# Performance work log

Hardware: AMD Instinct MI355X
Metric: run time of the kernel (lower is better)

## Reference

```python
import jax, jax.numpy as jnp
import numpy as np

B, S, DM = 4, 2048, 512
H, D = 8, 64          # att_head, head_dim = att_dim // att_head
LEFT, RIGHT = 128, 128  # band_part(left_mask, right_mask)
LARGE = 1e30          # masked_softmax large number for fp32


def setup_inputs() -> dict:
    key = jax.random.key(0)
    ks = jax.random.split(key, 11)
    scale = 1.0 / np.sqrt(DM)
    x = jax.random.normal(ks[0], (B, S, DM), jnp.float32)
    Wq = jax.random.normal(ks[1], (DM, DM), jnp.float32) * scale
    bq = jnp.zeros((DM,), jnp.float32)
    Wk = jax.random.normal(ks[2], (DM, DM), jnp.float32) * scale
    bk = jnp.zeros((DM,), jnp.float32)
    Wv = jax.random.normal(ks[3], (DM, DM), jnp.float32) * scale
    bv = jnp.zeros((DM,), jnp.float32)
    Wo = jax.random.normal(ks[4], (DM, DM), jnp.float32) * scale
    bo = jnp.zeros((DM,), jnp.float32)
    x_len = jax.random.randint(ks[5], (B,), 0, 2048)
    return {"x": x, "Wq": Wq, "bq": bq, "Wk": Wk, "bk": bk,
            "Wv": Wv, "bv": bv, "Wo": Wo, "bo": bo, "x_len": x_len}


def reference(x, Wq, bq, Wk, bk, Wv, bv, Wo, bo, x_len):
    b, s, _ = x.shape
    # QKV projections, split into heads: [B,S,H,D]
    q = (x @ Wq + bq).reshape(b, s, H, D)
    k = (x @ Wk + bk).reshape(b, s, H, D)
    v = (x @ Wv + bv).reshape(b, s, H, D)
    # content energy: [B,H,Q,K], scaled by sqrt(head_dim)
    energy = jnp.einsum('bind,bjnd->bnij', q, k) / jnp.sqrt(jnp.float32(D))
    # banded mask (tf.linalg.band_part semantics): keep -LEFT <= j-i <= RIGHT
    i = jnp.arange(s)[:, None]
    j = jnp.arange(s)[None, :]
    band = ((j - i) <= RIGHT) & ((i - j) <= LEFT)            # [S,S]
    # key-length mask (tf.sequence_mask, expanded to [B,1,1,S])
    seq = jnp.arange(s)[None, :] < x_len[:, None]            # [B,S]
    mask = (band[None, None, :, :] & seq[:, None, None, :]).astype(energy.dtype)
    # masked softmax: energy - (1 - mask) * LARGE, softmax over keys
    att = jax.nn.softmax(energy - (1.0 - mask) * LARGE, axis=-1)
    # context: [B,Q,H,D] -> [B,S,H*D]
    ctx = jnp.einsum('bnij,bjnd->bind', att, v).reshape(b, s, H * D)
    # output projection (use_proj=True)
    return ctx @ Wo + bo
```

## Files before the change

kernel.cpp:

```cpp
#include <hip/hip_runtime.h>

#define S_LEN 2048
#define BATCH 4
#define DMODEL 512
#define NHEAD 8
#define HDIM 64
#define ROWS (BATCH * S_LEN)

using short8 = __attribute__((ext_vector_type(8))) short;
using f32x4  = __attribute__((ext_vector_type(4))) float;

__device__ __forceinline__ unsigned short f2bf(float f) {
  unsigned int u = __builtin_bit_cast(unsigned int, f);
  u += 0x7fffu + ((u >> 16) & 1u);
  return (unsigned short)(u >> 16);
}
__device__ __forceinline__ float bf2f(unsigned short h) {
  unsigned int u = ((unsigned int)h) << 16;
  return __builtin_bit_cast(float, u);
}
__device__ __forceinline__ void glds16(const void* g, void* l) {
  __builtin_amdgcn_global_load_lds((const __attribute__((address_space(1))) unsigned*)g,
                                   (__attribute__((address_space(3))) unsigned*)l, 16, 0, 0);
}

__global__ __launch_bounds__(256) void prep_kernel(const float* __restrict__ x,
                                                   const float* __restrict__ Wq,
                                                   const float* __restrict__ Wk,
                                                   const float* __restrict__ Wv,
                                                   const float* __restrict__ Wo,
                                                   unsigned short* __restrict__ xb,
                                                   unsigned short* __restrict__ WqkT,
                                                   unsigned short* __restrict__ WvT,
                                                   unsigned short* __restrict__ WoT,
                                                   float* __restrict__ xpart) {
  __shared__ float t[32][33];
  const int blk = blockIdx.x, tid = threadIdx.x;
  if (blk < 2048) {
    const int base = (blk * 256 + tid) * 8;
    float4 f0 = *(const float4*)(x + base);
    float4 f1 = *(const float4*)(x + base + 4);
    uint4 o;
    o.x = (unsigned)f2bf(f0.x) | ((unsigned)f2bf(f0.y) << 16);
    o.y = (unsigned)f2bf(f0.z) | ((unsigned)f2bf(f0.w) << 16);
    o.z = (unsigned)f2bf(f1.x) | ((unsigned)f2bf(f1.y) << 16);
    o.w = (unsigned)f2bf(f1.z) | ((unsigned)f2bf(f1.w) << 16);
    *(uint4*)(xb + base) = o;
    return;
  }
  if (blk < 3072) {
    const int tb = blk - 2048;
    const int which = tb >> 8, tile = tb & 255;
    const float* W = which == 0 ? Wq : which == 1 ? Wk : which == 2 ? Wv : Wo;
    unsigned short* WT = which == 0 ? WqkT : which == 1 ? (WqkT + 512 * 512)
                        : which == 2 ? WvT : WoT;
    const int tx = tid & 31, ty = tid >> 5;
    const int x0 = (tile & 15) * 32, y0 = (tile >> 4) * 32;
#pragma unroll
    for (int r = 0; r < 4; r++)
      t[ty + 8 * r][tx] = W[(size_t)(y0 + ty + 8 * r) * DMODEL + x0 + tx];
    __syncthreads();
#pragma unroll
    for (int r = 0; r < 4; r++)
      WT[(size_t)(x0 + ty + 8 * r) * DMODEL + y0 + tx] = f2bf(t[tx][ty + 8 * r]);
    return;
  }
  const int u = blk - 3072;
  const int b = u >> 4, cg = (u >> 3) & 1, rc = u & 7;
  const float* base = x + (size_t)(b * S_LEN + rc * 256) * DMODEL + cg * 256 + tid;
  float s = 0.f;
  for (int j = 0; j < 256; j++) s += base[(size_t)j * DMODEL];
  xpart[u * 256 + tid] = s;
}

__global__ __launch_bounds__(256, 2) void qkv_kernel(const unsigned short* __restrict__ xb,
                                                     const unsigned short* __restrict__ WqkT,
                                                     const unsigned short* __restrict__ WvT,
                                                     const float* __restrict__ bq,
                                                     const float* __restrict__ bk,
                                                     const float* __restrict__ bv,
                                                     const int* __restrict__ x_len,
                                                     const float* __restrict__ xpart,
                                                     unsigned short* __restrict__ Qb,
                                                     unsigned short* __restrict__ Kb,
                                                     unsigned short* __restrict__ Vt,
                                                     float* __restrict__ vsum) {
  __shared__ __align__(16) char smem[32768];
  const int bid = blockIdx.x;
  const int tid = threadIdx.x;
  const int wave = tid >> 6, lane = tid & 63;
  if (bid >= 768) {
    const int u = bid - 768;
    const int b = u >> 5;
    const int cg = lane >> 5, ko = (lane & 31) * 8;
    float xs[8] = {};
#pragma unroll
    for (int rc = 0; rc < 8; rc++) {
      const float* p = xpart + ((b * 16 + cg * 8 + rc) << 8) + ko;
      float4 a0 = *(const float4*)p;
      float4 a1 = *(const float4*)(p + 4);
      xs[0] += a0.x; xs[1] += a0.y; xs[2] += a0.z; xs[3] += a0.w;
      xs[4] += a1.x; xs[5] += a1.y; xs[6] += a1.z; xs[7] += a1.w;
    }
#pragma unroll
    for (int ci = 0; ci < 4; ci++) {
      const int f = (u & 31) * 16 + wave * 4 + ci;
      const uint4 wv = *(const uint4*)(WvT + (size_t)f * DMODEL + lane * 8);
      const unsigned int w[4] = {wv.x, wv.y, wv.z, wv.w};
      float acc = 0.f;
#pragma unroll
      for (int e = 0; e < 4; e++) {
        acc += xs[2 * e] * bf2f((unsigned short)(w[e] & 0xffffu));
        acc += xs[2 * e + 1] * bf2f((unsigned short)(w[e] >> 16));
      }
#pragma unroll
      for (int off = 1; off < 64; off <<= 1) acc += __shfl_xor(acc, off, 64);
      if (lane == 0) vsum[b * DMODEL + f] = acc + 2048.f * bv[f];
    }
    return;
  }
  const bool vmode = bid < 256;
  const unsigned short *A, *Bt;
  int m0, n0;
  if (vmode) {
    m0 = (bid & 3) * 128;
    n0 = (bid >> 2) * 128;
    A = WvT; Bt = xb;
    if ((n0 & 2047) >= x_len[n0 >> 11]) return;
  } else {
    const int q = bid - 256;
    m0 = (q >> 3) * 128;
    n0 = (q & 7) * 128;
    A = xb; Bt = WqkT;
    const int xl = x_len[m0 >> 11];
    const int s0 = m0 & 2047;
    if (n0 >= DMODEL) { if (s0 >= xl) return; }
    else if (s0 >= xl + 128) return;
  }
  char* As = smem;
  char* Bs = smem + 16384;
  const int wr = wave >> 1, wc = wave & 1;
  const int lm = lane & 15, lq = lane >> 4;
  const int srow = lane >> 3;
  const int slc = (lane & 7) ^ (srow & 7);
  const unsigned short* gA[4];
  const unsigned short* gB[4];
  char *lA[4], *lB[4];
#pragma unroll
  for (int i = 0; i < 4; i++) {
    const int g = wave * 4 + i;
    gA[i] = A + (size_t)(m0 + g * 8 + srow) * DMODEL + slc * 8;
    gB[i] = Bt + (size_t)(n0 + g * 8 + srow) * DMODEL + slc * 8;
    lA[i] = As + g * 1024 + lane * 16;
    lB[i] = Bs + g * 1024 + lane * 16;
  }
  int aoff[4][2], boff[4][2];
#pragma unroll
  for (int mi = 0; mi < 4; mi++)
#pragma unroll
    for (int h = 0; h < 2; h++) {
      aoff[mi][h] = (wr * 64 + mi * 16 + lm) * 128 + ((((h << 2) | lq)) ^ (lm & 7)) * 16;
      boff[mi][h] = (wc * 64 + mi * 16 + lm) * 128 + ((((h << 2) | lq)) ^ (lm & 7)) * 16;
    }
  f32x4 acc[4][4] = {};
  for (int k0 = 0; k0 < DMODEL; k0 += 64) {
    __syncthreads();
#pragma unroll
    for (int i = 0; i < 4; i++) {
      glds16(gA[i] + k0, lA[i]);
      glds16(gB[i] + k0, lB[i]);
    }
    __syncthreads();
#pragma unroll
    for (int h = 0; h < 2; h++) {
      short8 af[4], bfr[4];
#pragma unroll
      for (int mi = 0; mi < 4; mi++) af[mi] = *(const short8*)(As + aoff[mi][h]);
#pragma unroll
      for (int ni = 0; ni < 4; ni++) bfr[ni] = *(const short8*)(Bs + boff[ni][h]);
#pragma unroll
      for (int mi = 0; mi < 4; mi++)
#pragma unroll
        for (int ni = 0; ni < 4; ni++)
          acc[mi][ni] = __builtin_amdgcn_mfma_f32_16x16x32_bf16(af[mi], bfr[ni], acc[mi][ni], 0, 0, 0);
    }
  }
#pragma unroll
  for (int mi = 0; mi < 4; mi++) {
    const int row0 = m0 + wr * 64 + mi * 16 + lq * 4;
#pragma unroll
    for (int ni = 0; ni < 4; ni++) {
      const int col = n0 + wc * 64 + ni * 16 + lm;
#pragma unroll
      for (int r = 0; r < 4; r++) {
        const int row = row0 + r;
        const float v = acc[mi][ni][r];
        if (vmode) {
          Vt[(size_t)row * ROWS + col] = f2bf(v + bv[row]);
        } else if (col < DMODEL) {
          Qb[(size_t)row * DMODEL + col] = f2bf(v + bq[col]);
        } else {
          Kb[(size_t)row * DMODEL + (col - DMODEL)] = f2bf(v + bk[col - DMODEL]);
        }
      }
    }
  }
}

__global__ __launch_bounds__(256) void attn_kernel(const unsigned short* __restrict__ Q,
                                                   const unsigned short* __restrict__ K,
                                                   const unsigned short* __restrict__ Vt,
                                                   const int* __restrict__ x_len,
                                                   const float* __restrict__ vsum,
                                                   const unsigned short* __restrict__ WoT,
                                                   const float* __restrict__ bo,
                                                   float* __restrict__ trow,
                                                   unsigned short* __restrict__ ctx) {
  __shared__ unsigned short Ks[64][72];
  __shared__ unsigned short Vs[64][72];
  __shared__ unsigned short Ps[4][16][72];
  const int tid = threadIdx.x;
  const int unit = blockIdx.x;
  const int wave = tid >> 6, lane = tid & 63;
  if (unit >= 1024) {
    const int u = unit - 1024;
    const int b = u >> 4;
    const float* vs = vsum + b * DMODEL + lane * 8;
    float vreg[8];
    *(float4*)vreg = *(const float4*)vs;
    *(float4*)(vreg + 4) = *(const float4*)(vs + 4);
#pragma unroll
    for (int ci = 0; ci < 8; ci++) {
      const int c = (u & 15) * 32 + wave * 8 + ci;
      const uint4 wv = *(const uint4*)(WoT + (size_t)c * DMODEL + lane * 8);
      const unsigned int w[4] = {wv.x, wv.y, wv.z, wv.w};
      float acc = 0.f;
#pragma unroll
      for (int e = 0; e < 4; e++) {
        acc += vreg[2 * e] * bf2f((unsigned short)(w[e] & 0xffffu));
        acc += vreg[2 * e + 1] * bf2f((unsigned short)(w[e] >> 16));
      }
#pragma unroll
      for (int off = 1; off < 64; off <<= 1) acc += __shfl_xor(acc, off, 64);
      if (lane == 0) trow[b * DMODEL + c] = bo[c] + acc * (1.f / 2048.f);
    }
    return;
  }
  const int b = unit >> 8, h = (unit >> 5) & 7;
  const int i0 = (unit & 31) * 64;
  const int xlen = x_len[b];
  const int t0 = min(S_LEN, xlen + 128);
  if ((i0 & ~127) >= t0) return;
  const int lm = lane & 15, lq = lane >> 4;
  const int q0 = i0 + wave * 16;
  const size_t qoff = (size_t)(b * S_LEN + q0 + lm) * DMODEL + h * HDIM + lq * 8;
  const short8 aq0 = *(const short8*)(Q + qoff);
  const short8 aq1 = *(const short8*)(Q + qoff + 32);
  const int sr = tid >> 3, sc = (tid & 7) * 8;
  f32x4 oacc[4] = {};
  float lrow[4] = {0.f, 0.f, 0.f, 0.f};
  for (int kt = 0; kt < 5; kt++) {
    const int jt0 = i0 - 128 + kt * 64;
    if (jt0 + 63 < 0 || jt0 >= xlen) continue;
    __syncthreads();
    {
      const int jr0 = min(max(jt0 + sr, 0), S_LEN - 1);
      const int jr1 = min(max(jt0 + sr + 32, 0), S_LEN - 1);
      *(uint4*)&Ks[sr][sc] =
          *(const uint4*)(K + (size_t)(b * S_LEN + jr0) * DMODEL + h * HDIM + sc);
      *(uint4*)&Ks[sr + 32][sc] =
          *(const uint4*)(K + (size_t)(b * S_LEN + jr1) * DMODEL + h * HDIM + sc);
      const int jvc = min(max(jt0 + sc, 0), S_LEN - 8);
      *(uint4*)&Vs[sr][sc] =
          *(const uint4*)(Vt + (size_t)(h * HDIM + sr) * ROWS + b * S_LEN + jvc);
      *(uint4*)&Vs[sr + 32][sc] =
          *(const uint4*)(Vt + (size_t)(h * HDIM + sr + 32) * ROWS + b * S_LEN + jvc);
    }
    __syncthreads();
    if (jt0 + 63 < q0 - 128 || jt0 > q0 + 143) continue;

    f32x4 sv[4];
#pragma unroll
    for (int sub = 0; sub < 4; sub++) {
      const short8 bk0 = *(const short8*)&Ks[sub * 16 + lm][lq * 8];
      const short8 bk1 = *(const short8*)&Ks[sub * 16 + lm][32 + lq * 8];
      f32x4 s = {};
      s = __builtin_amdgcn_mfma_f32_16x16x32_bf16(aq0, bk0, s, 0, 0, 0);
      s = __builtin_amdgcn_mfma_f32_16x16x32_bf16(aq1, bk1, s, 0, 0, 0);
      sv[sub] = s;
    }
    float p[4][4];
#pragma unroll
    for (int sub = 0; sub < 4; sub++) {
      const int j = jt0 + sub * 16 + lm;
      const bool jv = (j >= 0) && (j < xlen);
#pragma unroll
      for (int r = 0; r < 4; r++) {
        const int i = q0 + lq * 4 + r;
        const bool ok = jv && (j - i <= 128) && (i - j <= 128);
        const float pv = ok ? __expf(sv[sub][r] * 0.125f) : 0.f;
        p[sub][r] = pv;
        lrow[r] += pv;
      }
    }
#pragma unroll
    for (int sub = 0; sub < 4; sub++)
#pragma unroll
      for (int r = 0; r < 4; r++)
        Ps[wave][lq * 4 + r][sub * 16 + lm] = f2bf(p[sub][r]);
    const short8 pf0 = *(const short8*)&Ps[wave][lm][lq * 8];
    const short8 pf1 = *(const short8*)&Ps[wave][lm][32 + lq * 8];
#pragma unroll
    for (int dt = 0; dt < 4; dt++) {
      const short8 bv0 = *(const short8*)&Vs[dt * 16 + lm][lq * 8];
      const short8 bv1 = *(const short8*)&Vs[dt * 16 + lm][32 + lq * 8];
      oacc[dt] = __builtin_amdgcn_mfma_f32_16x16x32_bf16(pf0, bv0, oacc[dt], 0, 0, 0);
      oacc[dt] = __builtin_amdgcn_mfma_f32_16x16x32_bf16(pf1, bv1, oacc[dt], 0, 0, 0);
    }
  }
#pragma unroll
  for (int r = 0; r < 4; r++)
#pragma unroll
    for (int off = 1; off < 16; off <<= 1) lrow[r] += __shfl_xor(lrow[r], off, 64);
#pragma unroll
  for (int r = 0; r < 4; r++) {
    const int i = q0 + lq * 4 + r;
    const size_t obase = (size_t)(b * S_LEN + i) * DMODEL + h * HDIM;
    if (lrow[r] > 0.f) {
      const float inv = 1.f / lrow[r];
#pragma unroll
      for (int dt = 0; dt < 4; dt++)
        ctx[obase + dt * 16 + lm] = f2bf(oacc[dt][r] * inv);
    } else {
#pragma unroll
      for (int dt = 0; dt < 4; dt++)
        ctx[obase + dt * 16 + lm] =
            f2bf(vsum[(size_t)b * DMODEL + h * HDIM + dt * 16 + lm] * (1.f / 2048.f));
    }
  }
}

__global__ __launch_bounds__(256, 2) void out_kernel(const unsigned short* __restrict__ A,
                                                     const unsigned short* __restrict__ Bt,
                                                     const float* __restrict__ bias,
                                                     const int* __restrict__ x_len,
                                                     const float* __restrict__ trow,
                                                     float* __restrict__ out) {
  __shared__ __align__(16) char smem[32768];
  const int tid = threadIdx.x;
  const int m0 = (blockIdx.x >> 2) * 128, n0 = (blockIdx.x & 3) * 128;
  const int xl = x_len[m0 >> 11];
  if ((m0 & 2047) >= min(S_LEN, xl + 128)) {
    const float4 val = *(const float4*)(trow + (m0 >> 11) * DMODEL + n0 + (tid & 31) * 4);
    float* obase = out + (size_t)m0 * DMODEL + n0 + (tid & 31) * 4;
#pragma unroll
    for (int r = tid >> 5; r < 128; r += 8)
      *(float4*)(obase + (size_t)r * DMODEL) = val;
    return;
  }
  char* As = smem;
  char* Bs = smem + 16384;
  const int wave = tid >> 6, lane = tid & 63;
  const int wr = wave >> 1, wc = wave & 1;
  const int lm = lane & 15, lq = lane >> 4;
  const int srow = lane >> 3;
  const int slc = (lane & 7) ^ (srow & 7);
  const unsigned short* gA[4];
  const unsigned short* gB[4];
  char *lA[4], *lB[4];
#pragma unroll
  for (int i = 0; i < 4; i++) {
    const int g = wave * 4 + i;
    gA[i] = A + (size_t)(m0 + g * 8 + srow) * DMODEL + slc * 8;
    gB[i] = Bt + (size_t)(n0 + g * 8 + srow) * DMODEL + slc * 8;
    lA[i] = As + g * 1024 + lane * 16;
    lB[i] = Bs + g * 1024 + lane * 16;
  }
  int aoff[4][2], boff[4][2];
#pragma unroll
  for (int mi = 0; mi < 4; mi++)
#pragma unroll
    for (int h = 0; h < 2; h++) {
      aoff[mi][h] = (wr * 64 + mi * 16 + lm) * 128 + ((((h << 2) | lq)) ^ (lm & 7)) * 16;
      boff[mi][h] = (wc * 64 + mi * 16 + lm) * 128 + ((((h << 2) | lq)) ^ (lm & 7)) * 16;
    }
  f32x4 acc[4][4] = {};
  for (int k0 = 0; k0 < DMODEL; k0 += 64) {
    __syncthreads();
#pragma unroll
    for (int i = 0; i < 4; i++) {
      glds16(gA[i] + k0, lA[i]);
      glds16(gB[i] + k0, lB[i]);
    }
    __syncthreads();
#pragma unroll
    for (int h = 0; h < 2; h++) {
      short8 af[4], bfr[4];
#pragma unroll
      for (int mi = 0; mi < 4; mi++) af[mi] = *(const short8*)(As + aoff[mi][h]);
#pragma unroll
      for (int ni = 0; ni < 4; ni++) bfr[ni] = *(const short8*)(Bs + boff[ni][h]);
#pragma unroll
      for (int mi = 0; mi < 4; mi++)
#pragma unroll
        for (int ni = 0; ni < 4; ni++)
          acc[mi][ni] = __builtin_amdgcn_mfma_f32_16x16x32_bf16(af[mi], bfr[ni], acc[mi][ni], 0, 0, 0);
    }
  }
#pragma unroll
  for (int mi = 0; mi < 4; mi++) {
    const int row0 = m0 + wr * 64 + mi * 16 + lq * 4;
#pragma unroll
    for (int ni = 0; ni < 4; ni++) {
      const int col = n0 + wc * 64 + ni * 16 + lm;
#pragma unroll
      for (int r = 0; r < 4; r++)
        out[(size_t)(row0 + r) * DMODEL + col] = acc[mi][ni][r] + bias[col];
    }
  }
}

extern "C" void kernel_launch(void* const* d_in, const int* in_sizes, int n_in,
                              void* d_out, int out_size, void* d_ws, size_t ws_size,
                              hipStream_t stream) {
  (void)in_sizes; (void)n_in; (void)out_size; (void)ws_size;
  const float* x  = (const float*)d_in[0];
  const float* Wq = (const float*)d_in[1];
  const float* bq = (const float*)d_in[2];
  const float* Wk = (const float*)d_in[3];
  const float* bk = (const float*)d_in[4];
  const float* Wv = (const float*)d_in[5];
  const float* bv = (const float*)d_in[6];
  const float* Wo = (const float*)d_in[7];
  const float* bo = (const float*)d_in[8];
  const int* x_len = (const int*)d_in[9];

  char* ws = (char*)d_ws;
  const size_t MB = 1024 * 1024;
  unsigned short* xb   = (unsigned short*)(ws + 0 * MB);
  unsigned short* Qb   = (unsigned short*)(ws + 8 * MB);
  unsigned short* Kb   = (unsigned short*)(ws + 16 * MB);
  unsigned short* Vt   = (unsigned short*)(ws + 24 * MB);
  unsigned short* Cx   = (unsigned short*)(ws + 32 * MB);
  unsigned short* WqkT = (unsigned short*)(ws + 40 * MB);
  unsigned short* WvT  = (unsigned short*)(ws + 41 * MB);
  unsigned short* WoT  = (unsigned short*)(ws + 41 * MB + 512 * 1024);
  float* vsum          = (float*)(ws + 42 * MB);
  float* trow          = (float*)(ws + 42 * MB + 8192);
  float* xpart         = (float*)(ws + 43 * MB);

  prep_kernel<<<3136, 256, 0, stream>>>(x, Wq, Wk, Wv, Wo, xb, WqkT, WvT, WoT, xpart);
  qkv_kernel<<<896, 256, 0, stream>>>(xb, WqkT, WvT, bq, bk, bv, x_len, xpart,
                                      Qb, Kb, Vt, vsum);
  attn_kernel<<<1088, 256, 0, stream>>>(Qb, Kb, Vt, x_len, vsum, WoT, bo, trow, Cx);
  out_kernel<<<256, 256, 0, stream>>>(Cx, WoT, bo, x_len, trow, (float*)d_out);
}
```

Measured before the change: 146.8 us.

## Double-buffer GEMM and attention K/V tiles to overlap loads with MFMA

The QKV and output GEMMs now use a K-step of 32 with two shared-memory buffers, so the next tile's global-to-LDS loads are issued before the MFMAs on the current tile, and there is one barrier per step instead of two. The attention kernel double-buffers K and V tiles, prefetching the next tile into registers while computing on the current one, and computes the valid key-tile range up front instead of skipping tiles inside the loop. qkv launch bounds are raised to 3 blocks per CU. The change hides memory latency at the cost of more LDS and register use and a new swizzle that must stay correct.

```diff
diff --git a/kernel.cpp b/kernel.cpp
--- a/kernel.cpp
+++ b/kernel.cpp
@@ -73,7 +73,7 @@
   xpart[u * 256 + tid] = s;
 }
 
-__global__ __launch_bounds__(256, 2) void qkv_kernel(const unsigned short* __restrict__ xb,
+__global__ __launch_bounds__(256, 3) void qkv_kernel(const unsigned short* __restrict__ xb,
                                                      const unsigned short* __restrict__ WqkT,
                                                      const unsigned short* __restrict__ WvT,
                                                      const float* __restrict__ bq,
@@ -137,53 +137,50 @@
     if (n0 >= DMODEL) { if (s0 >= xl) return; }
     else if (s0 >= xl + 128) return;
   }
-  char* As = smem;
-  char* Bs = smem + 16384;
   const int wr = wave >> 1, wc = wave & 1;
   const int lm = lane & 15, lq = lane >> 4;
-  const int srow = lane >> 3;
-  const int slc = (lane & 7) ^ (srow & 7);
-  const unsigned short* gA[4];
-  const unsigned short* gB[4];
-  char *lA[4], *lB[4];
-#pragma unroll
-  for (int i = 0; i < 4; i++) {
-    const int g = wave * 4 + i;
-    gA[i] = A + (size_t)(m0 + g * 8 + srow) * DMODEL + slc * 8;
-    gB[i] = Bt + (size_t)(n0 + g * 8 + srow) * DMODEL + slc * 8;
-    lA[i] = As + g * 1024 + lane * 16;
-    lB[i] = Bs + g * 1024 + lane * 16;
-  }
-  int aoff[4][2], boff[4][2];
-#pragma unroll
-  for (int mi = 0; mi < 4; mi++)
-#pragma unroll
-    for (int h = 0; h < 2; h++) {
-      aoff[mi][h] = (wr * 64 + mi * 16 + lm) * 128 + ((((h << 2) | lq)) ^ (lm & 7)) * 16;
-      boff[mi][h] = (wc * 64 + mi * 16 + lm) * 128 + ((((h << 2) | lq)) ^ (lm & 7)) * 16;
-    }
+  const int r4 = tid >> 2;
+  const int cl = (tid & 3) ^ ((tid >> 3) & 3);
+  const unsigned short* ga0 = A + (size_t)(m0 + r4) * DMODEL + cl * 8;
+  const unsigned short* ga1 = ga0 + (size_t)64 * DMODEL;
+  const unsigned short* gb0 = Bt + (size_t)(n0 + r4) * DMODEL + cl * 8;
+  const unsigned short* gb1 = gb0 + (size_t)64 * DMODEL;
+  char* la0 = smem + tid * 16;
+  char* lb0 = smem + 16384 + tid * 16;
+  const int phys = (lq ^ ((lm >> 1) & 3)) * 16;
+  int aoff[4], boff[4];
+#pragma unroll
+  for (int mi = 0; mi < 4; mi++) {
+    aoff[mi] = (wr * 64 + mi * 16 + lm) * 64 + phys;
+    boff[mi] = (wc * 64 + mi * 16 + lm) * 64 + phys;
+  }
   f32x4 acc[4][4] = {};
-  for (int k0 = 0; k0 < DMODEL; k0 += 64) {
-    __syncthreads();
-#pragma unroll
-    for (int i = 0; i < 4; i++) {
-      glds16(gA[i] + k0, lA[i]);
-      glds16(gB[i] + k0, lB[i]);
-    }
-    __syncthreads();
-#pragma unroll
-    for (int h = 0; h < 2; h++) {
-      short8 af[4], bfr[4];
-#pragma unroll
-      for (int mi = 0; mi < 4; mi++) af[mi] = *(const short8*)(As + aoff[mi][h]);
-#pragma unroll
-      for (int ni = 0; ni < 4; ni++) bfr[ni] = *(const short8*)(Bs + boff[ni][h]);
-#pragma unroll
-      for (int mi = 0; mi < 4; mi++)
-#pragma unroll
-        for (int ni = 0; ni < 4; ni++)
-          acc[mi][ni] = __builtin_amdgcn_mfma_f32_16x16x32_bf16(af[mi], bfr[ni], acc[mi][ni], 0, 0, 0);
-    }
+  glds16(ga0, la0);
+  glds16(ga1, la0 + 4096);
+  glds16(gb0, lb0);
+  glds16(gb1, lb0 + 4096);
+  __syncthreads();
+#pragma unroll
+  for (int it = 0; it < 16; ++it) {
+    if (it < 15) {
+      const int nb = ((it + 1) & 1) << 13;
+      glds16(ga0 + (it + 1) * 32, la0 + nb);
+      glds16(ga1 + (it + 1) * 32, la0 + nb + 4096);
+      glds16(gb0 + (it + 1) * 32, lb0 + nb);
+      glds16(gb1 + (it + 1) * 32, lb0 + nb + 4096);
+    }
+    const int ab = (it & 1) << 13;
+    short8 af[4], bfr[4];
+#pragma unroll
+    for (int mi = 0; mi < 4; mi++) af[mi] = *(const short8*)(smem + ab + aoff[mi]);
+#pragma unroll
+    for (int ni = 0; ni < 4; ni++) bfr[ni] = *(const short8*)(smem + 16384 + ab + boff[ni]);
+#pragma unroll
+    for (int mi = 0; mi < 4; mi++)
+#pragma unroll
+      for (int ni = 0; ni < 4; ni++)
+        acc[mi][ni] = __builtin_amdgcn_mfma_f32_16x16x32_bf16(af[mi], bfr[ni], acc[mi][ni], 0, 0, 0);
+    if (it < 15) __syncthreads();
   }
 #pragma unroll
   for (int mi = 0; mi < 4; mi++) {
@@ -216,8 +213,8 @@
                                                    const float* __restrict__ bo,
                                                    float* __restrict__ trow,
                                                    unsigned short* __restrict__ ctx) {
-  __shared__ unsigned short Ks[64][72];
-  __shared__ unsigned short Vs[64][72];
+  __shared__ unsigned short Ks[2][64][72];
+  __shared__ unsigned short Vs[2][64][72];
   __shared__ unsigned short Ps[4][16][72];
   const int tid = threadIdx.x;
   const int unit = blockIdx.x;
@@ -259,63 +256,86 @@
   const int sr = tid >> 3, sc = (tid & 7) * 8;
   f32x4 oacc[4] = {};
   float lrow[4] = {0.f, 0.f, 0.f, 0.f};
-  for (int kt = 0; kt < 5; kt++) {
-    const int jt0 = i0 - 128 + kt * 64;
-    if (jt0 + 63 < 0 || jt0 >= xlen) continue;
-    __syncthreads();
+  const int ktlo = (i0 >= 128) ? 0 : ((i0 >= 64) ? 1 : 2);
+  const int kthi = min(5, (xlen + 128 - i0 + 63) >> 6);
+  if (ktlo < kthi) {
     {
+      const int jt0 = i0 - 128 + ktlo * 64;
       const int jr0 = min(max(jt0 + sr, 0), S_LEN - 1);
       const int jr1 = min(max(jt0 + sr + 32, 0), S_LEN - 1);
-      *(uint4*)&Ks[sr][sc] =
+      const int jvc = min(max(jt0 + sc, 0), S_LEN - 8);
+      const int p = ktlo & 1;
+      *(uint4*)&Ks[p][sr][sc] =
           *(const uint4*)(K + (size_t)(b * S_LEN + jr0) * DMODEL + h * HDIM + sc);
-      *(uint4*)&Ks[sr + 32][sc] =
+      *(uint4*)&Ks[p][sr + 32][sc] =
           *(const uint4*)(K + (size_t)(b * S_LEN + jr1) * DMODEL + h * HDIM + sc);
-      const int jvc = min(max(jt0 + sc, 0), S_LEN - 8);
-      *(uint4*)&Vs[sr][sc] =
+      *(uint4*)&Vs[p][sr][sc] =
           *(const uint4*)(Vt + (size_t)(h * HDIM + sr) * ROWS + b * S_LEN + jvc);
-      *(uint4*)&Vs[sr + 32][sc] =
+      *(uint4*)&Vs[p][sr + 32][sc] =
           *(const uint4*)(Vt + (size_t)(h * HDIM + sr + 32) * ROWS + b * S_LEN + jvc);
     }
     __syncthreads();
-    if (jt0 + 63 < q0 - 128 || jt0 > q0 + 143) continue;
-
-    f32x4 sv[4];
-#pragma unroll
-    for (int sub = 0; sub < 4; sub++) {
-      const short8 bk0 = *(const short8*)&Ks[sub * 16 + lm][lq * 8];
-      const short8 bk1 = *(const short8*)&Ks[sub * 16 + lm][32 + lq * 8];
-      f32x4 s = {};
-      s = __builtin_amdgcn_mfma_f32_16x16x32_bf16(aq0, bk0, s, 0, 0, 0);
-      s = __builtin_amdgcn_mfma_f32_16x16x32_bf16(aq1, bk1, s, 0, 0, 0);
-      sv[sub] = s;
-    }
-    float p[4][4];
-#pragma unroll
-    for (int sub = 0; sub < 4; sub++) {
-      const int j = jt0 + sub * 16 + lm;
-      const bool jv = (j >= 0) && (j < xlen);
-#pragma unroll
-      for (int r = 0; r < 4; r++) {
-        const int i = q0 + lq * 4 + r;
-        const bool ok = jv && (j - i <= 128) && (i - j <= 128);
-        const float pv = ok ? __expf(sv[sub][r] * 0.125f) : 0.f;
-        p[sub][r] = pv;
-        lrow[r] += pv;
-      }
-    }
-#pragma unroll
-    for (int sub = 0; sub < 4; sub++)
-#pragma unroll
-      for (int r = 0; r < 4; r++)
-        Ps[wave][lq * 4 + r][sub * 16 + lm] = f2bf(p[sub][r]);
-    const short8 pf0 = *(const short8*)&Ps[wave][lm][lq * 8];
-    const short8 pf1 = *(const short8*)&Ps[wave][lm][32 + lq * 8];
-#pragma unroll
-    for (int dt = 0; dt < 4; dt++) {
-      const short8 bv0 = *(const short8*)&Vs[dt * 16 + lm][lq * 8];
-      const short8 bv1 = *(const short8*)&Vs[dt * 16 + lm][32 + lq * 8];
-      oacc[dt] = __builtin_amdgcn_mfma_f32_16x16x32_bf16(pf0, bv0, oacc[dt], 0, 0, 0);
-      oacc[dt] = __builtin_amdgcn_mfma_f32_16x16x32_bf16(pf1, bv1, oacc[dt], 0, 0, 0);
+    for (int kt = ktlo; kt < kthi; kt++) {
+      const int p = kt & 1;
+      const int jt0 = i0 - 128 + kt * 64;
+      const bool more = (kt + 1 < kthi);
+      uint4 nk0, nk1, nv0, nv1;
+      if (more) {
+        const int njt0 = jt0 + 64;
+        const int jr0 = min(max(njt0 + sr, 0), S_LEN - 1);
+        const int jr1 = min(max(njt0 + sr + 32, 0), S_LEN - 1);
+        const int jvc = min(max(njt0 + sc, 0), S_LEN - 8);
+        nk0 = *(const uint4*)(K + (size_t)(b * S_LEN + jr0) * DMODEL + h * HDIM + sc);
+        nk1 = *(const uint4*)(K + (size_t)(b * S_LEN + jr1) * DMODEL + h * HDIM + sc);
+        nv0 = *(const uint4*)(Vt + (size_t)(h * HDIM + sr) * ROWS + b * S_LEN + jvc);
+        nv1 = *(const uint4*)(Vt + (size_t)(h * HDIM + sr + 32) * ROWS + b * S_LEN + jvc);
+      }
+      f32x4 sv[4];
+#pragma unroll
+      for (int sub = 0; sub < 4; sub++) {
+        const short8 bk0 = *(const short8*)&Ks[p][sub * 16 + lm][lq * 8];
+        const short8 bk1 = *(const short8*)&Ks[p][sub * 16 + lm][32 + lq * 8];
+        f32x4 s = {};
+        s = __builtin_amdgcn_mfma_f32_16x16x32_bf16(aq0, bk0, s, 0, 0, 0);
+        s = __builtin_amdgcn_mfma_f32_16x16x32_bf16(aq1, bk1, s, 0, 0, 0);
+        sv[sub] = s;
+      }
+      float pp[4][4];
+#pragma unroll
+      for (int sub = 0; sub < 4; sub++) {
+        const int j = jt0 + sub * 16 + lm;
+        const bool jv = (j >= 0) && (j < xlen);
+#pragma unroll
+        for (int r = 0; r < 4; r++) {
+          const int i = q0 + lq * 4 + r;
+          const bool ok = jv && (j - i <= 128) && (i - j <= 128);
+          const float pv = ok ? __expf(sv[sub][r] * 0.125f) : 0.f;
+          pp[sub][r] = pv;
+          lrow[r] += pv;
+        }
+      }
+#pragma unroll
+      for (int sub = 0; sub < 4; sub++)
+#pragma unroll
+        for (int r = 0; r < 4; r++)
+          Ps[wave][lq * 4 + r][sub * 16 + lm] = f2bf(pp[sub][r]);
+      const short8 pf0 = *(const short8*)&Ps[wave][lm][lq * 8];
+      const short8 pf1 = *(const short8*)&Ps[wave][lm][32 + lq * 8];
+#pragma unroll
+      for (int dt = 0; dt < 4; dt++) {
+        const short8 bv0 = *(const short8*)&Vs[p][dt * 16 + lm][lq * 8];
+        const short8 bv1 = *(const short8*)&Vs[p][dt * 16 + lm][32 + lq * 8];
+        oacc[dt] = __builtin_amdgcn_mfma_f32_16x16x32_bf16(pf0, bv0, oacc[dt], 0, 0, 0);
+        oacc[dt] = __builtin_amdgcn_mfma_f32_16x16x32_bf16(pf1, bv1, oacc[dt], 0, 0, 0);
+      }
+      if (more) {
+        const int np = p ^ 1;
+        *(uint4*)&Ks[np][sr][sc] = nk0;
+        *(uint4*)&Ks[np][sr + 32][sc] = nk1;
+        *(uint4*)&Vs[np][sr][sc] = nv0;
+        *(uint4*)&Vs[np][sr + 32][sc] = nv1;
+        __syncthreads();
+      }
     }
   }
 #pragma unroll
@@ -358,54 +378,51 @@
       *(float4*)(obase + (size_t)r * DMODEL) = val;
     return;
   }
-  char* As = smem;
-  char* Bs = smem + 16384;
   const int wave = tid >> 6, lane = tid & 63;
   const int wr = wave >> 1, wc = wave & 1;
   const int lm = lane & 15, lq = lane >> 4;
-  const int srow = lane >> 3;
-  const int slc = (lane & 7) ^ (srow & 7);
-  const unsigned short* gA[4];
-  const unsigned short* gB[4];
-  char *lA[4], *lB[4];
-#pragma unroll
-  for (int i = 0; i < 4; i++) {
-    const int g = wave * 4 + i;
-    gA[i] = A + (size_t)(m0 + g * 8 + srow) * DMODEL + slc * 8;
-    gB[i] = Bt + (size_t)(n0 + g * 8 + srow) * DMODEL + slc * 8;
-    lA[i] = As + g * 1024 + lane * 16;
-    lB[i] = Bs + g * 1024 + lane * 16;
-  }
-  int aoff[4][2], boff[4][2];
-#pragma unroll
-  for (int mi = 0; mi < 4; mi++)
-#pragma unroll
-    for (int h = 0; h < 2; h++) {
-      aoff[mi][h] = (wr * 64 + mi * 16 + lm) * 128 + ((((h << 2) | lq)) ^ (lm & 7)) * 16;
-      boff[mi][h] = (wc * 64 + mi * 16 + lm) * 128 + ((((h << 2) | lq)) ^ (lm & 7)) * 16;
-    }
+  const int r4 = tid >> 2;
+  const int cl = (tid & 3) ^ ((tid >> 3) & 3);
+  const unsigned short* ga0 = A + (size_t)(m0 + r4) * DMODEL + cl * 8;
+  const unsigned short* ga1 = ga0 + (size_t)64 * DMODEL;
+  const unsigned short* gb0 = Bt + (size_t)(n0 + r4) * DMODEL + cl * 8;
+  const unsigned short* gb1 = gb0 + (size_t)64 * DMODEL;
+  char* la0 = smem + tid * 16;
+  char* lb0 = smem + 16384 + tid * 16;
+  const int phys = (lq ^ ((lm >> 1) & 3)) * 16;
+  int aoff[4], boff[4];
+#pragma unroll
+  for (int mi = 0; mi < 4; mi++) {
+    aoff[mi] = (wr * 64 + mi * 16 + lm) * 64 + phys;
+    boff[mi] = (wc * 64 + mi * 16 + lm) * 64 + phys;
+  }
   f32x4 acc[4][4] = {};
-  for (int k0 = 0; k0 < DMODEL; k0 += 64) {
-    __syncthreads();
-#pragma unroll
-    for (int i = 0; i < 4; i++) {
-      glds16(gA[i] + k0, lA[i]);
-      glds16(gB[i] + k0, lB[i]);
-    }
-    __syncthreads();
-#pragma unroll
-    for (int h = 0; h < 2; h++) {
-      short8 af[4], bfr[4];
-#pragma unroll
-      for (int mi = 0; mi < 4; mi++) af[mi] = *(const short8*)(As + aoff[mi][h]);
-#pragma unroll
-      for (int ni = 0; ni < 4; ni++) bfr[ni] = *(const short8*)(Bs + boff[ni][h]);
-#pragma unroll
-      for (int mi = 0; mi < 4; mi++)
-#pragma unroll
-        for (int ni = 0; ni < 4; ni++)
-          acc[mi][ni] = __builtin_amdgcn_mfma_f32_16x16x32_bf16(af[mi], bfr[ni], acc[mi][ni], 0, 0, 0);
-    }
+  glds16(ga0, la0);
+  glds16(ga1, la0 + 4096);
+  glds16(gb0, lb0);
+  glds16(gb1, lb0 + 4096);
+  __syncthreads();
+#pragma unroll
+  for (int it = 0; it < 16; ++it) {
+    if (it < 15) {
+      const int nb = ((it + 1) & 1) << 13;
+      glds16(ga0 + (it + 1) * 32, la0 + nb);
+      glds16(ga1 + (it + 1) * 32, la0 + nb + 4096);
+      glds16(gb0 + (it + 1) * 32, lb0 + nb);
+      glds16(gb1 + (it + 1) * 32, lb0 + nb + 4096);
+    }
+    const int ab = (it & 1) << 13;
+    short8 af[4], bfr[4];
+#pragma unroll
+    for (int mi = 0; mi < 4; mi++) af[mi] = *(const short8*)(smem + ab + aoff[mi]);
+#pragma unroll
+    for (int ni = 0; ni < 4; ni++) bfr[ni] = *(const short8*)(smem + 16384 + ab + boff[ni]);
+#pragma unroll
+    for (int mi = 0; mi < 4; mi++)
+#pragma unroll
+      for (int ni = 0; ni < 4; ni++)
+        acc[mi][ni] = __builtin_amdgcn_mfma_f32_16x16x32_bf16(af[mi], bfr[ni], acc[mi][ni], 0, 0, 0);
+    if (it < 15) __syncthreads();
   }
 #pragma unroll
   for (int mi = 0; mi < 4; mi++) {
```

Measured after the change: 149.4 us. About the same (+1.8%).
